# Optimization experiments

Measured on AMD Instinct MI355X. Metric: run time of the kernel, lower is better.

## Reference

```python
import jax, jax.numpy as jnp
import numpy as np

H = 256  # hidden_units
B = 64   # batch
D = 2048 # question length


def setup_inputs() -> dict:
    key = jax.random.key(0)
    ks = jax.random.split(key, 9)
    s = 1.0 / np.sqrt(H)
    return {
        "context": jax.random.normal(ks[0], (B, H), dtype=jnp.float32),
        "question": jax.random.normal(ks[1], (B, D, H), dtype=jnp.float32),
        "hidden": jax.random.normal(ks[2], (1, B, H), dtype=jnp.float32),
        "W1": jax.random.uniform(ks[3], (H, H), jnp.float32, -s, s),  # linear_g1, no bias
        "W2": jax.random.uniform(ks[4], (H, H), jnp.float32, -s, s),  # linear_g2
        "b2": jax.random.uniform(ks[5], (H,), jnp.float32, -s, s),
        "W3": jax.random.uniform(ks[6], (H, H), jnp.float32, -s, s),  # linear_g3, no bias
        "W4": jax.random.uniform(ks[7], (1, H), jnp.float32, -s, s),  # linear_g4
        "b4": jax.random.uniform(ks[8], (1,), jnp.float32, -s, s),
    }


def reference(context, question, hidden, W1, W2, b2, W3, W4, b4):
    # hidden: (1,B,H) -> (B,1,H); linear_g3 (no bias)
    g3 = jnp.swapaxes(hidden, 0, 1) @ W3.T            # (B,1,H)
    # linear_g2 on context, then unsqueeze(1)
    g2 = (context @ W2.T + b2)[:, None, :]            # (B,1,H)
    # linear_g1 on question (no bias)
    g1 = question @ W1.T                              # (B,D,H)
    # The torch repeat/view sequence is exactly a broadcast add in (B,D,H)
    s = jnp.tanh(g2 + g3 + g1)                        # (B,D,H)
    scores = s @ W4.T + b4                            # (B,D,1)
    attn = jax.nn.softmax(scores, axis=1)             # softmax over D
    # attn.transpose(1,2) bmm question -> (B,1,H)
    return jnp.einsum('bdo,bdh->boh', attn, question)
```

## Files before the change

kernel.cpp:

```cpp
#include <hip/hip_runtime.h>
#include <hip/hip_bf16.h>
#include <math.h>

#define HD 256
#define BB 64
#define DD 2048
#define NCHK 4
#define NST 8

typedef __attribute__((ext_vector_type(8))) short  short8;
typedef __attribute__((ext_vector_type(4))) float  float4v;
typedef __attribute__((ext_vector_type(4))) unsigned uint4v;
typedef __attribute__((ext_vector_type(4))) unsigned short ushort4v;

__device__ inline unsigned short f2bf(float f) {
    unsigned u = __builtin_bit_cast(unsigned, f);
    u += 0x7FFFu + ((u >> 16) & 1u);
    return (unsigned short)(u >> 16);
}
__device__ inline float bf2f(unsigned short u) {
    return __builtin_bit_cast(float, (unsigned)u << 16);
}

__device__ inline short8 cvt8(float4v lo, float4v hi) {
    uint4v u;
    asm("v_cvt_pk_bf16_f32 %0, %1, %2" : "=v"(u[0]) : "v"(lo[0]), "v"(lo[1]));
    asm("v_cvt_pk_bf16_f32 %0, %1, %2" : "=v"(u[1]) : "v"(lo[2]), "v"(lo[3]));
    asm("v_cvt_pk_bf16_f32 %0, %1, %2" : "=v"(u[2]) : "v"(hi[0]), "v"(hi[1]));
    asm("v_cvt_pk_bf16_f32 %0, %1, %2" : "=v"(u[3]) : "v"(hi[2]), "v"(hi[3]));
    return __builtin_bit_cast(short8, u);
}

__device__ inline float fast_exp2(float x) {
    float r;
    asm("v_exp_f32 %0, %1" : "=v"(r) : "v"(x));
    return r;
}
__device__ inline float fast_tanh(float x) {
    float y = x * 2.8853900817779268f;
    y = fminf(fmaxf(y, -30.f), 30.f);
    float t = fast_exp2(y);
    float r;
    asm("v_rcp_f32 %0, %1" : "=v"(r) : "v"(t + 1.f));
    return (t - 1.f) * r;
}

#define SYNC_LDS() do { asm volatile("s_waitcnt lgkmcnt(0)" ::: "memory"); \
                        __builtin_amdgcn_s_barrier(); \
                        asm volatile("" ::: "memory"); } while (0)

__global__ __launch_bounds__(256) void k_prep(const float* __restrict__ W1,
                                              unsigned short* __restrict__ w1b,
                                              const float* __restrict__ ctx,
                                              const float* __restrict__ hid,
                                              const float* __restrict__ W2,
                                              const float* __restrict__ b2,
                                              const float* __restrict__ W3,
                                              float* __restrict__ g23) {
    if (blockIdx.x < 64) {
        int i = blockIdx.x * 256 + threadIdx.x;
        float4v v = ((const float4v*)W1)[i];
        ushort4v o;
        o[0] = f2bf(v[0]); o[1] = f2bf(v[1]); o[2] = f2bf(v[2]); o[3] = f2bf(v[3]);
        ((ushort4v*)w1b)[i] = o;
    } else {
        int b = blockIdx.x - 64, t = threadIdx.x;
        __shared__ float c[HD], hh[HD];
        c[t]  = ctx[b * HD + t];
        hh[t] = hid[b * HD + t];
        __syncthreads();
        const float4v* w2 = (const float4v*)(W2 + (size_t)t * HD);
        const float4v* w3 = (const float4v*)(W3 + (size_t)t * HD);
        float acc = b2[t];
        #pragma unroll 8
        for (int k = 0; k < 64; ++k) {
            float4v a = w2[k], d = w3[k];
            int k4 = k * 4;
            acc += c[k4] * a[0] + c[k4 + 1] * a[1] + c[k4 + 2] * a[2] + c[k4 + 3] * a[3];
            acc += hh[k4] * d[0] + hh[k4 + 1] * d[1] + hh[k4 + 2] * d[2] + hh[k4 + 3] * d[3];
        }
        g23[b * HD + t] = acc;
    }
}

__global__ __launch_bounds__(512) void k_fused(const float* __restrict__ q,
                                               const unsigned short* __restrict__ w1b,
                                               const float* __restrict__ g23,
                                               const float* __restrict__ W4,
                                               float* __restrict__ pl,
                                               float* __restrict__ pO) {
    __shared__ __attribute__((aligned(16))) unsigned short tile[64 * HD];
    __shared__ __attribute__((aligned(16))) unsigned short spb[64][8];

    const int t = threadIdx.x;
    const int chunk = blockIdx.x, b = blockIdx.y;
    const int lane = t & 63, wave = t >> 6;
    const int l15 = lane & 15, lk = lane >> 4;
    const int hb = wave * 32;
    const int cg = lane & 7, ro = lane >> 3;

    const float* qc = q + ((size_t)b * DD + chunk * 512) * HD;

    const int srow = t >> 5, schk = t & 31;
    const int swz = (srow & 7) << 4;

    float4v s0, s1, s2, s3, s4, s5, s6, s7;
    {
        const float* p0 = qc + (size_t)srow * HD + schk * 8;
        s0 = *(const float4v*)(p0);                s1 = *(const float4v*)(p0 + 4);
        s2 = *(const float4v*)(p0 + 16 * HD);      s3 = *(const float4v*)(p0 + 16 * HD + 4);
        s4 = *(const float4v*)(p0 + 32 * HD);      s5 = *(const float4v*)(p0 + 32 * HD + 4);
        s6 = *(const float4v*)(p0 + 48 * HD);      s7 = *(const float4v*)(p0 + 48 * HD + 4);
    }

    short8 bfr[8][2];
    #pragma unroll
    for (int kb = 0; kb < 8; ++kb)
        #pragma unroll
        for (int nf = 0; nf < 2; ++nf)
            bfr[kb][nf] = *(const short8*)&w1b[(size_t)(hb + nf * 16 + l15) * HD + kb * 32 + lk * 8];

    float gv[2][4], wv[2][4];
    #pragma unroll
    for (int nf = 0; nf < 2; ++nf)
        #pragma unroll
        for (int r = 0; r < 4; ++r) {
            int h = hb + nf * 16 + lk * 4 + r;
            gv[nf][r] = g23[b * HD + h];
            wv[nf][r] = W4[h];
        }

    float l = 0.f;
    float4v O = {0.f, 0.f, 0.f, 0.f};

    #pragma unroll 1
    for (int ts = 0; ts < NST; ++ts) {
        SYNC_LDS();

        {
            short8 p0 = cvt8(s0, s1);
            short8 p1 = cvt8(s2, s3);
            short8 p2 = cvt8(s4, s5);
            short8 p3 = cvt8(s6, s7);
            int base = srow * 512 + ((schk * 16) ^ swz);
            *(short8*)((char*)tile + base)              = p0;
            *(short8*)((char*)tile + base + 16 * 512)   = p1;
            *(short8*)((char*)tile + base + 32 * 512)   = p2;
            *(short8*)((char*)tile + base + 48 * 512)   = p3;
        }
        if (ts + 1 < NST) {
            const float* pn = qc + (size_t)((ts + 1) * 64 + srow) * HD + schk * 8;
            s0 = *(const float4v*)(pn);                s1 = *(const float4v*)(pn + 4);
            s2 = *(const float4v*)(pn + 16 * HD);      s3 = *(const float4v*)(pn + 16 * HD + 4);
            s4 = *(const float4v*)(pn + 32 * HD);      s5 = *(const float4v*)(pn + 32 * HD + 4);
            s6 = *(const float4v*)(pn + 48 * HD);      s7 = *(const float4v*)(pn + 48 * HD + 4);
        }
        SYNC_LDS();

        #pragma unroll
        for (int mf = 0; mf < 4; ++mf) {
            float4v acc0 = {0.f, 0.f, 0.f, 0.f}, acc1 = {0.f, 0.f, 0.f, 0.f};
            const int d = mf * 16 + l15;
            const int dsw = (d & 7) << 4;
            #pragma unroll
            for (int kb = 0; kb < 8; ++kb) {
                int byte = d * 512 + ((kb * 64 + lk * 16) ^ dsw);
                short8 bq = *(const short8*)((const char*)tile + byte);
                acc0 = __builtin_amdgcn_mfma_f32_16x16x32_bf16(bfr[kb][0], bq, acc0, 0, 0, 0);
                acc1 = __builtin_amdgcn_mfma_f32_16x16x32_bf16(bfr[kb][1], bq, acc1, 0, 0, 0);
            }
            float s = 0.f;
            #pragma unroll
            for (int r = 0; r < 4; ++r) s += fast_tanh(acc0[r] + gv[0][r]) * wv[0][r];
            #pragma unroll
            for (int r = 0; r < 4; ++r) s += fast_tanh(acc1[r] + gv[1][r]) * wv[1][r];
            s += __shfl_xor(s, 16, 64);
            s += __shfl_xor(s, 32, 64);
            if (lk == 0) spb[mf * 16 + l15][wave] = f2bf(s);
        }
        SYNC_LDS();

        float sc;
        {
            ushort4v a = *(const ushort4v*)&spb[lane][0];
            ushort4v c = *(const ushort4v*)&spb[lane][4];
            sc = bf2f(a[0]) + bf2f(a[1]) + bf2f(a[2]) + bf2f(a[3])
               + bf2f(c[0]) + bf2f(c[1]) + bf2f(c[2]) + bf2f(c[3]);
        }
        float w = fast_exp2(sc * 1.4426950408889634f);
        l += w;
        const int cb = wave * 64 + cg * 8;
        #pragma unroll
        for (int i = 0; i < 8; ++i) {
            int d = ro * 8 + i;
            float wd = __shfl(w, d, 64);
            int byte = d * 512 + (cb ^ ((d & 7) << 4));
            ushort4v v = *(const ushort4v*)((const char*)tile + byte);
            O[0] += wd * bf2f(v[0]);
            O[1] += wd * bf2f(v[1]);
            O[2] += wd * bf2f(v[2]);
            O[3] += wd * bf2f(v[3]);
        }
    }

    #pragma unroll
    for (int j = 0; j < 4; ++j) {
        O[j] += __shfl_xor(O[j], 8, 64);
        O[j] += __shfl_xor(O[j], 16, 64);
        O[j] += __shfl_xor(O[j], 32, 64);
    }
    if (ro == 0)
        *(float4v*)&pO[((size_t)(b * NCHK + chunk)) * HD + wave * 32 + cg * 4] = O;

    l += __shfl_xor(l, 1, 64);
    l += __shfl_xor(l, 2, 64);
    l += __shfl_xor(l, 4, 64);
    l += __shfl_xor(l, 8, 64);
    l += __shfl_xor(l, 16, 64);
    l += __shfl_xor(l, 32, 64);
    if (t == 0) pl[b * NCHK + chunk] = l;
}

__global__ __launch_bounds__(256) void k_comb(const float* __restrict__ pl,
                                              const float* __restrict__ pO,
                                              float* __restrict__ out) {
    int b = blockIdx.x, t = threadIdx.x;
    float L = 0.f;
    #pragma unroll
    for (int c = 0; c < NCHK; ++c) L += pl[b * NCHK + c];
    float s = 0.f;
    #pragma unroll
    for (int c = 0; c < NCHK; ++c) s += pO[((size_t)(b * NCHK + c)) * HD + t];
    out[b * HD + t] = s / L;
}

extern "C" void kernel_launch(void* const* d_in, const int* in_sizes, int n_in,
                              void* d_out, int out_size, void* d_ws, size_t ws_size,
                              hipStream_t stream) {
    (void)in_sizes; (void)n_in; (void)out_size; (void)ws_size;
    const float* ctx = (const float*)d_in[0];
    const float* q   = (const float*)d_in[1];
    const float* hid = (const float*)d_in[2];
    const float* W1  = (const float*)d_in[3];
    const float* W2  = (const float*)d_in[4];
    const float* b2  = (const float*)d_in[5];
    const float* W3  = (const float*)d_in[6];
    const float* W4  = (const float*)d_in[7];
    float* out = (float*)d_out;

    char* ws = (char*)d_ws;
    unsigned short* w1b = (unsigned short*)(ws);
    float* g23 = (float*)(ws + 131072);
    float* pl  = (float*)(ws + 196608);
    float* pO  = (float*)(ws + 197632);

    k_prep <<<dim3(128), dim3(256), 0, stream>>>(W1, w1b, ctx, hid, W2, b2, W3, g23);
    k_fused<<<dim3(NCHK, BB), dim3(512), 0, stream>>>(q, w1b, g23, W4, pl, pO);
    k_comb <<<dim3(BB), dim3(256), 0, stream>>>(pl, pO, out);
}
```

Measured before the change: 63.28 us.

## Double work-group to 1024 threads, split rows across waves, double-buffer LDS tile

Each fused work-group now runs 16 waves instead of 8. Two wave groups each own half of the 64 question rows in a tile, for both the MFMA score pass and the weighted sum. The converted tile now alternates between two LDS buffers, which removes the barrier at the top of each step. The g23 and W4 vectors move into LDS, and the partial outputs of the two wave halves are combined through a small LDS array before being written. The aim is better latency hiding and fewer barriers per tile, at the cost of double the LDS, a 128-VGPR cap per thread that could cause spills, and one extra reduction step.

```diff
diff --git a/kernel.cpp b/kernel.cpp
--- a/kernel.cpp
+++ b/kernel.cpp
@@ -83,34 +83,35 @@
     }
 }
 
-__global__ __launch_bounds__(512) void k_fused(const float* __restrict__ q,
-                                               const unsigned short* __restrict__ w1b,
-                                               const float* __restrict__ g23,
-                                               const float* __restrict__ W4,
-                                               float* __restrict__ pl,
-                                               float* __restrict__ pO) {
-    __shared__ __attribute__((aligned(16))) unsigned short tile[64 * HD];
+__global__ __launch_bounds__(1024) void k_fused(const float* __restrict__ q,
+                                                const unsigned short* __restrict__ w1b,
+                                                const float* __restrict__ g23,
+                                                const float* __restrict__ W4,
+                                                float* __restrict__ pl,
+                                                float* __restrict__ pO) {
+    __shared__ __attribute__((aligned(16))) unsigned short buf0[64 * HD];
+    __shared__ __attribute__((aligned(16))) unsigned short buf1[64 * HD];
     __shared__ __attribute__((aligned(16))) unsigned short spb[64][8];
+    __shared__ float g23s[HD], w4s[HD];
+    __shared__ float oacc[16][32];
 
     const int t = threadIdx.x;
     const int chunk = blockIdx.x, b = blockIdx.y;
     const int lane = t & 63, wave = t >> 6;
     const int l15 = lane & 15, lk = lane >> 4;
-    const int hb = wave * 32;
-    const int cg = lane & 7, ro = lane >> 3;
+    const int hg = wave & 7, dh = wave >> 3;
+    const int hb = hg * 32;
 
     const float* qc = q + ((size_t)b * DD + chunk * 512) * HD;
 
     const int srow = t >> 5, schk = t & 31;
     const int swz = (srow & 7) << 4;
 
-    float4v s0, s1, s2, s3, s4, s5, s6, s7;
+    float4v s0, s1, s2, s3;
     {
         const float* p0 = qc + (size_t)srow * HD + schk * 8;
-        s0 = *(const float4v*)(p0);                s1 = *(const float4v*)(p0 + 4);
-        s2 = *(const float4v*)(p0 + 16 * HD);      s3 = *(const float4v*)(p0 + 16 * HD + 4);
-        s4 = *(const float4v*)(p0 + 32 * HD);      s5 = *(const float4v*)(p0 + 32 * HD + 4);
-        s6 = *(const float4v*)(p0 + 48 * HD);      s7 = *(const float4v*)(p0 + 48 * HD + 4);
+        s0 = *(const float4v*)(p0);            s1 = *(const float4v*)(p0 + 4);
+        s2 = *(const float4v*)(p0 + 32 * HD);  s3 = *(const float4v*)(p0 + 32 * HD + 4);
     }
 
     short8 bfr[8][2];
@@ -120,63 +121,58 @@
         for (int nf = 0; nf < 2; ++nf)
             bfr[kb][nf] = *(const short8*)&w1b[(size_t)(hb + nf * 16 + l15) * HD + kb * 32 + lk * 8];
 
-    float gv[2][4], wv[2][4];
-    #pragma unroll
-    for (int nf = 0; nf < 2; ++nf)
-        #pragma unroll
-        for (int r = 0; r < 4; ++r) {
-            int h = hb + nf * 16 + lk * 4 + r;
-            gv[nf][r] = g23[b * HD + h];
-            wv[nf][r] = W4[h];
-        }
+    if (t < 256)      g23s[t] = g23[b * HD + t];
+    else if (t < 512) w4s[t - 256] = W4[t - 256];
 
     float l = 0.f;
     float4v O = {0.f, 0.f, 0.f, 0.f};
 
     #pragma unroll 1
     for (int ts = 0; ts < NST; ++ts) {
-        SYNC_LDS();
+        unsigned short* cur = (ts & 1) ? buf1 : buf0;
 
         {
             short8 p0 = cvt8(s0, s1);
             short8 p1 = cvt8(s2, s3);
-            short8 p2 = cvt8(s4, s5);
-            short8 p3 = cvt8(s6, s7);
             int base = srow * 512 + ((schk * 16) ^ swz);
-            *(short8*)((char*)tile + base)              = p0;
-            *(short8*)((char*)tile + base + 16 * 512)   = p1;
-            *(short8*)((char*)tile + base + 32 * 512)   = p2;
-            *(short8*)((char*)tile + base + 48 * 512)   = p3;
+            *(short8*)((char*)cur + base)            = p0;
+            *(short8*)((char*)cur + base + 32 * 512) = p1;
         }
         if (ts + 1 < NST) {
             const float* pn = qc + (size_t)((ts + 1) * 64 + srow) * HD + schk * 8;
-            s0 = *(const float4v*)(pn);                s1 = *(const float4v*)(pn + 4);
-            s2 = *(const float4v*)(pn + 16 * HD);      s3 = *(const float4v*)(pn + 16 * HD + 4);
-            s4 = *(const float4v*)(pn + 32 * HD);      s5 = *(const float4v*)(pn + 32 * HD + 4);
-            s6 = *(const float4v*)(pn + 48 * HD);      s7 = *(const float4v*)(pn + 48 * HD + 4);
+            s0 = *(const float4v*)(pn);            s1 = *(const float4v*)(pn + 4);
+            s2 = *(const float4v*)(pn + 32 * HD);  s3 = *(const float4v*)(pn + 32 * HD + 4);
         }
         SYNC_LDS();
 
         #pragma unroll
-        for (int mf = 0; mf < 4; ++mf) {
+        for (int mf = 0; mf < 2; ++mf) {
             float4v acc0 = {0.f, 0.f, 0.f, 0.f}, acc1 = {0.f, 0.f, 0.f, 0.f};
-            const int d = mf * 16 + l15;
+            const int d = dh * 32 + mf * 16 + l15;
             const int dsw = (d & 7) << 4;
             #pragma unroll
             for (int kb = 0; kb < 8; ++kb) {
                 int byte = d * 512 + ((kb * 64 + lk * 16) ^ dsw);
-                short8 bq = *(const short8*)((const char*)tile + byte);
+                short8 bq = *(const short8*)((const char*)cur + byte);
                 acc0 = __builtin_amdgcn_mfma_f32_16x16x32_bf16(bfr[kb][0], bq, acc0, 0, 0, 0);
                 acc1 = __builtin_amdgcn_mfma_f32_16x16x32_bf16(bfr[kb][1], bq, acc1, 0, 0, 0);
             }
             float s = 0.f;
-            #pragma unroll
-            for (int r = 0; r < 4; ++r) s += fast_tanh(acc0[r] + gv[0][r]) * wv[0][r];
-            #pragma unroll
-            for (int r = 0; r < 4; ++r) s += fast_tanh(acc1[r] + gv[1][r]) * wv[1][r];
+            {
+                float4v g4 = *(const float4v*)&g23s[hb + lk * 4];
+                float4v w4 = *(const float4v*)&w4s[hb + lk * 4];
+                #pragma unroll
+                for (int r = 0; r < 4; ++r) s += fast_tanh(acc0[r] + g4[r]) * w4[r];
+            }
+            {
+                float4v g4 = *(const float4v*)&g23s[hb + 16 + lk * 4];
+                float4v w4 = *(const float4v*)&w4s[hb + 16 + lk * 4];
+                #pragma unroll
+                for (int r = 0; r < 4; ++r) s += fast_tanh(acc1[r] + g4[r]) * w4[r];
+            }
             s += __shfl_xor(s, 16, 64);
             s += __shfl_xor(s, 32, 64);
-            if (lk == 0) spb[mf * 16 + l15][wave] = f2bf(s);
+            if (lk == 0) spb[dh * 32 + mf * 16 + l15][hg] = f2bf(s);
         }
         SYNC_LDS();
 
@@ -189,13 +185,13 @@
         }
         float w = fast_exp2(sc * 1.4426950408889634f);
         l += w;
-        const int cb = wave * 64 + cg * 8;
+        const int cwb = hg * 64 + (lane & 7) * 8;
         #pragma unroll
-        for (int i = 0; i < 8; ++i) {
-            int d = ro * 8 + i;
+        for (int i = 0; i < 4; ++i) {
+            int d = dh * 32 + (lane >> 3) * 4 + i;
             float wd = __shfl(w, d, 64);
-            int byte = d * 512 + (cb ^ ((d & 7) << 4));
-            ushort4v v = *(const ushort4v*)((const char*)tile + byte);
+            int byte = d * 512 + (cwb ^ ((d & 7) << 4));
+            ushort4v v = *(const ushort4v*)((const char*)cur + byte);
             O[0] += wd * bf2f(v[0]);
             O[1] += wd * bf2f(v[1]);
             O[2] += wd * bf2f(v[2]);
@@ -209,9 +205,14 @@
         O[j] += __shfl_xor(O[j], 16, 64);
         O[j] += __shfl_xor(O[j], 32, 64);
     }
-    if (ro == 0)
-        *(float4v*)&pO[((size_t)(b * NCHK + chunk)) * HD + wave * 32 + cg * 4] = O;
-
+    SYNC_LDS();
+    if (lane < 8)
+        *(float4v*)&oacc[wave][(lane & 7) * 4] = O;
+    SYNC_LDS();
+    if (t < 256) {
+        float o = oacc[t >> 5][t & 31] + oacc[(t >> 5) + 8][t & 31];
+        pO[((size_t)(b * NCHK + chunk)) * HD + t] = o;
+    }
     l += __shfl_xor(l, 1, 64);
     l += __shfl_xor(l, 2, 64);
     l += __shfl_xor(l, 4, 64);
@@ -255,6 +256,6 @@
     float* pO  = (float*)(ws + 197632);
 
     k_prep <<<dim3(128), dim3(256), 0, stream>>>(W1, w1b, ctx, hid, W2, b2, W3, g23);
-    k_fused<<<dim3(NCHK, BB), dim3(512), 0, stream>>>(q, w1b, g23, W4, pl, pO);
+    k_fused<<<dim3(NCHK, BB), dim3(1024), 0, stream>>>(q, w1b, g23, W4, pl, pO);
     k_comb <<<dim3(BB), dim3(256), 0, stream>>>(pl, pO, out);
 }
```

After: 121.2 us. 91.5% more time.
